# Performance work log

Hardware: AMD Instinct MI355X
Metric: run time of the kernel (lower is better)

Reference implementation:

```python
import jax, jax.numpy as jnp
import numpy as np

B, I, T = 8192, 128, 21
H1, H2, H3 = 256, 256, 128


def _init(key, shape, fan_in):
    # torch-style uniform(-1/sqrt(fan_in), 1/sqrt(fan_in))
    bound = 1.0 / np.sqrt(fan_in)
    return jax.random.uniform(key, shape, jnp.float32, -bound, bound)


def setup_inputs() -> dict:
    key = jax.random.key(0)
    ks = jax.random.split(key, 16)
    x = jax.random.normal(ks[0], (B, I, T), jnp.float32)
    d = {"x": x}
    # stacked LSTM weights (PyTorch layout: W_ih (4H, in), gate order i,f,g,o)
    d["W1_ih"] = _init(ks[1], (4 * H1, I), H1)
    d["b1_ih"] = _init(ks[2], (4 * H1,), H1)
    d["b1_hh"] = _init(ks[3], (4 * H1,), H1)
    d["W2_ih"] = _init(ks[4], (4 * H2, H1), H2)
    d["b2_ih"] = _init(ks[5], (4 * H2,), H2)
    d["b2_hh"] = _init(ks[6], (4 * H2,), H2)
    d["W3_ih"] = _init(ks[7], (4 * H3, H2), H3)
    d["b3_ih"] = _init(ks[8], (4 * H3,), H3)
    d["b3_hh"] = _init(ks[9], (4 * H3,), H3)
    d["fc1_w"] = _init(ks[10], (1, H3), H3)
    d["fc1_b"] = _init(ks[11], (1,), H3)
    d["fc2_w"] = _init(ks[12], (T, T), T)
    d["fc2_b"] = _init(ks[13], (T,), T)
    return d


def _lstm_cell_step(xt, W_ih, b_ih, b_hh):
    # single timestep with h0 = c0 = 0, so the W_hh @ h0 term vanishes
    gates = xt @ W_ih.T + (b_ih + b_hh)          # (B, 21, 4H)
    i, f, g, o = jnp.split(gates, 4, axis=-1)    # torch gate order i,f,g,o
    c = jax.nn.sigmoid(i) * jnp.tanh(g)          # f * c0 = 0
    return jax.nn.sigmoid(o) * jnp.tanh(c)


def reference(x, W1_ih, b1_ih, b1_hh, W2_ih, b2_ih, b2_hh,
              W3_ih, b3_ih, b3_hh, fc1_w, fc1_b, fc2_w, fc2_b):
    # fold the 21 independent single-step columns into the batch dim
    xt = jnp.transpose(x, (0, 2, 1))             # (B, 21, I)
    h1 = _lstm_cell_step(xt, W1_ih, b1_ih, b1_hh)   # (B, 21, H1)
    h2 = _lstm_cell_step(h1, W2_ih, b2_ih, b2_hh)   # (B, 21, H2)
    h3 = _lstm_cell_step(h2, W3_ih, b3_ih, b3_hh)   # (B, 21, H3)
    y = h3 @ fc1_w.T + fc1_b                     # (B, 21, 1)
    y = y[..., 0][:, None, :]                    # (B, 1, 21)  == x_torch
    out = y @ fc2_w.T + fc2_b                    # (B, 1, 21)
    return out
```

## Files before the change

### kernel.cpp

```cpp
#include <hip/hip_runtime.h>
#include <hip/hip_bf16.h>
#include <stdint.h>


typedef __attribute__((ext_vector_type(8))) short bf16x8;
typedef __attribute__((ext_vector_type(4))) float f32x4;

#define M_ROWS 172032
#define BATCH  8192

__device__ __forceinline__ float bf2f(unsigned short u) {
    union { unsigned int i; float f; } v; v.i = ((unsigned int)u) << 16; return v.f;
}
__device__ __forceinline__ unsigned short f2bf(float f) {
    union { float f; unsigned int i; } v; v.f = f;
    unsigned int r = v.i + 0x7fffu + ((v.i >> 16) & 1u);
    return (unsigned short)(r >> 16);
}
__device__ __forceinline__ float sigmoidf_(float x) {
    return __builtin_amdgcn_rcpf(1.0f + __expf(-x));
}
__device__ __forceinline__ float tanhf_(float x) {
    x = fminf(fmaxf(x, -20.0f), 20.0f);
    float e = __expf(-2.0f * x);
    return (1.0f - e) * __builtin_amdgcn_rcpf(1.0f + e);
}
__device__ __forceinline__ void g2l16(const unsigned short* g, unsigned short* l) {
    __builtin_amdgcn_global_load_lds(
        (const __attribute__((address_space(1))) unsigned int*)g,
        (__attribute__((address_space(3))) unsigned int*)l, 16, 0, 0);
}

__global__ __launch_bounds__(256) void k_convert(
    const float* __restrict__ src, unsigned short* __restrict__ dst, int n4)
{
    int i = blockIdx.x * 256 + threadIdx.x;
    if (i < n4) {
        float4 v = ((const float4*)src)[i];
        ushort4 o;
        o.x = f2bf(v.x); o.y = f2bf(v.y); o.z = f2bf(v.z); o.w = f2bf(v.w);
        ((ushort4*)dst)[i] = o;
    }
}

__global__ __launch_bounds__(256) void k_transpose(
    const float* __restrict__ x, unsigned short* __restrict__ xt)
{
    __shared__ unsigned short tile[128 * 22];
    const int b = blockIdx.x, tid = threadIdx.x;
    const float* xb = x + (size_t)b * 2688;
    for (int idx = tid; idx < 2688; idx += 256) {
        int i = idx / 21, t = idx - i * 21;
        tile[i * 22 + t] = f2bf(xb[idx]);
    }
    __syncthreads();
    unsigned short* xtb = xt + (size_t)b * 2688;
    for (int idx = tid; idx < 2688; idx += 256) {
        int t = idx >> 7, i = idx & 127;
        xtb[t * 128 + i] = tile[i * 22 + t];
    }
}

template<int K, int HG>
__global__ __launch_bounds__(256, 2) void k_gemm_act(
    const unsigned short* __restrict__ A,
    const unsigned short* __restrict__ W,
    const float* __restrict__ bih,
    const float* __restrict__ bhh,
    unsigned short* __restrict__ Hout)
{
    __shared__ __align__(16) unsigned short As[128 * 64];
    __shared__ __align__(16) unsigned short Ws[192 * 64];
    __shared__ float Bs[192];

    const int tid  = threadIdx.x;
    const int wave = tid >> 6;
    const int lane = tid & 63;
    const int wm = wave >> 1;
    const int wn = wave & 1;
    const int c0 = blockIdx.x * 64;
    const int r0 = blockIdx.y * 128;

    if (tid < 192) {
        int g = tid >> 6, c = tid & 63;
        int gbase = (g == 0) ? 0 : (g + 1) * HG;
        int idx = gbase + c0 + c;
        Bs[tid] = bih[idx] + bhh[idx];
    }

    f32x4 acc[3][4][2];
#pragma unroll
    for (int g = 0; g < 3; ++g)
#pragma unroll
        for (int m = 0; m < 4; ++m)
#pragma unroll
            for (int n = 0; n < 2; ++n)
                acc[g][m][n] = (f32x4){0.f, 0.f, 0.f, 0.f};

    const int l_hi = lane >> 3;
    const int l_lo = (lane & 7) * 8;

#pragma unroll
    for (int kk = 0; kk < K; kk += 64) {
        if (kk) __syncthreads();
#pragma unroll
        for (int i = 0; i < 4; ++i) {
            int row = wave * 32 + i * 8;
            g2l16(A + (size_t)(r0 + row + l_hi) * K + kk + l_lo, &As[row * 64]);
        }
#pragma unroll
        for (int i = 0; i < 6; ++i) {
            int row  = wave * 48 + i * 8;
            int lrow = row + l_hi;
            int gate = lrow >> 6;
            int n    = lrow & 63;
            int gbase = (gate == 0) ? 0 : (gate + 1) * HG;
            g2l16(W + (size_t)(gbase + c0 + n) * K + kk + l_lo, &Ws[row * 64]);
        }
        __syncthreads();

#pragma unroll
        for (int ks = 0; ks < 64; ks += 32) {
            bf16x8 af[4];
            bf16x8 bfr[3][2];
            const int koff = ks + (lane >> 4) * 8;
            const int rsel = lane & 15;
#pragma unroll
            for (int m = 0; m < 4; ++m)
                af[m] = *(const bf16x8*)&As[(wm * 64 + m * 16 + rsel) * 64 + koff];
#pragma unroll
            for (int g = 0; g < 3; ++g)
#pragma unroll
                for (int n = 0; n < 2; ++n)
                    bfr[g][n] = *(const bf16x8*)&Ws[(g * 64 + wn * 32 + n * 16 + rsel) * 64 + koff];
#pragma unroll
            for (int g = 0; g < 3; ++g)
#pragma unroll
                for (int m = 0; m < 4; ++m)
#pragma unroll
                    for (int n = 0; n < 2; ++n)
                        acc[g][m][n] = __builtin_amdgcn_mfma_f32_16x16x32_bf16(
                            af[m], bfr[g][n], acc[g][m][n], 0, 0, 0);
        }
    }

    const int quad = lane >> 4;
    const int csel = lane & 15;
#pragma unroll
    for (int m = 0; m < 4; ++m) {
#pragma unroll
        for (int n = 0; n < 2; ++n) {
            int cloc = wn * 32 + n * 16 + csel;
            float bi = Bs[cloc], bg = Bs[64 + cloc], bo = Bs[128 + cloc];
            f32x4 vi = acc[0][m][n], vg = acc[1][m][n], vo = acc[2][m][n];
#pragma unroll
            for (int r = 0; r < 4; ++r) {
                int row = r0 + wm * 64 + m * 16 + quad * 4 + r;
                float cv = sigmoidf_(vi[r] + bi) * tanhf_(vg[r] + bg);
                float h  = sigmoidf_(vo[r] + bo) * tanhf_(cv);
                Hout[(size_t)row * HG + c0 + cloc] = f2bf(h);
            }
        }
    }
}

#define FSTR 169
__global__ __launch_bounds__(256) void k_final(
    const unsigned short* __restrict__ h3,
    const float* __restrict__ fc1w,
    const float* __restrict__ fc1b,
    const float* __restrict__ fc2w,
    const float* __restrict__ fc2b,
    float* __restrict__ out)
{
    __shared__ unsigned short ht[128 * FSTR];
    __shared__ float fwl[128];
    __shared__ float yl[168];
    __shared__ float f2l[441];
    __shared__ float f2bl[21];

    const int tid = threadIdx.x;
    const int b0 = blockIdx.x * 8;

    if (tid < 128) fwl[tid] = fc1w[tid];
    for (int i = tid; i < 441; i += 256) f2l[i] = fc2w[i];
    if (tid < 21) f2bl[tid] = fc2b[tid];

    const unsigned int* hsrc = (const unsigned int*)(h3 + (size_t)b0 * 2688);
    for (int gi = tid; gi < 10752; gi += 256) {
        unsigned int v = hsrc[gi];
        int e = gi * 2;
        int task = e >> 7;
        int c = e & 127;
        ht[c * FSTR + task] = (unsigned short)(v & 0xffffu);
        ht[(c + 1) * FSTR + task] = (unsigned short)(v >> 16);
    }
    __syncthreads();

    const float f1b = fc1b[0];
    if (tid < 168) {
        float s = f1b;
#pragma unroll 8
        for (int c = 0; c < 128; ++c)
            s += fwl[c] * bf2f(ht[c * FSTR + tid]);
        yl[tid] = s;
    }
    __syncthreads();
    if (tid < 168) {
        int bloc = tid / 21;
        int tp = tid - bloc * 21;
        float s = f2bl[tp];
#pragma unroll
        for (int t = 0; t < 21; ++t)
            s += yl[bloc * 21 + t] * f2l[tp * 21 + t];
        out[(size_t)(b0 + bloc) * 21 + tp] = s;
    }
}

extern "C" void kernel_launch(void* const* d_in, const int* in_sizes, int n_in,
                              void* d_out, int out_size, void* d_ws, size_t ws_size,
                              hipStream_t stream)
{
    const float* x    = (const float*)d_in[0];
    const float* W1   = (const float*)d_in[1];
    const float* b1i  = (const float*)d_in[2];
    const float* b1h  = (const float*)d_in[3];
    const float* W2   = (const float*)d_in[4];
    const float* b2i  = (const float*)d_in[5];
    const float* b2h  = (const float*)d_in[6];
    const float* W3   = (const float*)d_in[7];
    const float* b3i  = (const float*)d_in[8];
    const float* b3h  = (const float*)d_in[9];
    const float* fc1w = (const float*)d_in[10];
    const float* fc1b = (const float*)d_in[11];
    const float* fc2w = (const float*)d_in[12];
    const float* fc2b = (const float*)d_in[13];
    float* out = (float*)d_out;

    unsigned short* Wc1 = (unsigned short*)d_ws;
    unsigned short* Wc2 = Wc1 + 131072;
    unsigned short* Wc3 = Wc2 + 262144;
    unsigned short* buf = Wc3 + 131072;

    int C = 1;
    while (C < 64 && 1048576 + (size_t)(M_ROWS / C) * 1536 > ws_size) C <<= 1;
    const int R  = M_ROWS / C;
    const int Bc = BATCH / C;

    unsigned short* xt = buf;
    unsigned short* h1 = xt + (size_t)R * 128;
    unsigned short* h2 = h1 + (size_t)R * 256;
    unsigned short* h3 = h2 + (size_t)R * 256;

    k_convert<<<128, 256, 0, stream>>>(W1, Wc1, 32768);
    k_convert<<<256, 256, 0, stream>>>(W2, Wc2, 65536);
    k_convert<<<128, 256, 0, stream>>>(W3, Wc3, 32768);

    for (int c = 0; c < C; ++c) {
        const float* xc = x + (size_t)c * Bc * 2688;
        k_transpose<<<Bc, 256, 0, stream>>>(xc, xt);
        k_gemm_act<128, 256><<<dim3(4, R / 128), 256, 0, stream>>>(xt, Wc1, b1i, b1h, h1);
        k_gemm_act<256, 256><<<dim3(4, R / 128), 256, 0, stream>>>(h1, Wc2, b2i, b2h, h2);
        k_gemm_act<256, 128><<<dim3(2, R / 128), 256, 0, stream>>>(h2, Wc3, b3i, b3h, h3);
        k_final<<<Bc / 8, 256, 0, stream>>>(h3, fc1w, fc1b, fc2w, fc2b,
                                            out + (size_t)c * Bc * 21);
    }
}
```

Before: 442.1 us.

## Fuse three LSTM layers and fc1 into one kernel with LDS-resident activations

```diff
diff --git a/kernel.cpp b/kernel.cpp
--- a/kernel.cpp
+++ b/kernel.cpp
@@ -62,77 +62,57 @@
 }
 
 template<int K, int HG>
-__global__ __launch_bounds__(256, 2) void k_gemm_act(
-    const unsigned short* __restrict__ A,
+__device__ __forceinline__ void gemm_layer(
+    const unsigned short* hin, unsigned short* hout,
     const unsigned short* __restrict__ W,
-    const float* __restrict__ bih,
-    const float* __restrict__ bhh,
-    unsigned short* __restrict__ Hout)
-{
-    __shared__ __align__(16) unsigned short As[128 * 64];
-    __shared__ __align__(16) unsigned short Ws[192 * 64];
-    __shared__ float Bs[192];
-
-    const int tid  = threadIdx.x;
-    const int wave = tid >> 6;
-    const int lane = tid & 63;
-    const int wm = wave >> 1;
-    const int wn = wave & 1;
-    const int c0 = blockIdx.x * 64;
-    const int r0 = blockIdx.y * 128;
-
-    if (tid < 192) {
-        int g = tid >> 6, c = tid & 63;
-        int gbase = (g == 0) ? 0 : (g + 1) * HG;
-        int idx = gbase + c0 + c;
-        Bs[tid] = bih[idx] + bhh[idx];
-    }
-
-    f32x4 acc[3][4][2];
-#pragma unroll
-    for (int g = 0; g < 3; ++g)
-#pragma unroll
-        for (int m = 0; m < 4; ++m)
-#pragma unroll
-            for (int n = 0; n < 2; ++n)
-                acc[g][m][n] = (f32x4){0.f, 0.f, 0.f, 0.f};
-
-    const int l_hi = lane >> 3;
-    const int l_lo = (lane & 7) * 8;
-
-#pragma unroll
-    for (int kk = 0; kk < K; kk += 64) {
-        if (kk) __syncthreads();
-#pragma unroll
-        for (int i = 0; i < 4; ++i) {
-            int row = wave * 32 + i * 8;
-            g2l16(A + (size_t)(r0 + row + l_hi) * K + kk + l_lo, &As[row * 64]);
+    const float* __restrict__ bih, const float* __restrict__ bhh,
+    int wave, int lane)
+{
+    const int quad = lane >> 4;
+    const int rsel = lane & 15;
+    const int r7   = rsel & 7;
+
+#pragma unroll
+    for (int pass = 0; pass < HG / 128; ++pass) {
+        const int c0 = pass * 128 + wave * 32;
+
+        float bias[3][2];
+#pragma unroll
+        for (int g = 0; g < 3; ++g) {
+            int gb = (g == 0) ? 0 : (g + 1) * HG;
+#pragma unroll
+            for (int n = 0; n < 2; ++n) {
+                int idx = gb + c0 + n * 16 + rsel;
+                bias[g][n] = bih[idx] + bhh[idx];
+            }
         }
-#pragma unroll
-        for (int i = 0; i < 6; ++i) {
-            int row  = wave * 48 + i * 8;
-            int lrow = row + l_hi;
-            int gate = lrow >> 6;
-            int n    = lrow & 63;
-            int gbase = (gate == 0) ? 0 : (gate + 1) * HG;
-            g2l16(W + (size_t)(gbase + c0 + n) * K + kk + l_lo, &Ws[row * 64]);
-        }
-        __syncthreads();
-
-#pragma unroll
-        for (int ks = 0; ks < 64; ks += 32) {
+
+        f32x4 acc[3][4][2];
+#pragma unroll
+        for (int g = 0; g < 3; ++g)
+#pragma unroll
+            for (int m = 0; m < 4; ++m)
+#pragma unroll
+                for (int n = 0; n < 2; ++n)
+                    acc[g][m][n] = (f32x4){0.f, 0.f, 0.f, 0.f};
+
+#pragma unroll
+        for (int ks = 0; ks < K / 32; ++ks) {
             bf16x8 af[4];
+            const int gsw = (ks * 4 + quad) ^ r7;
+#pragma unroll
+            for (int m = 0; m < 4; ++m)
+                af[m] = *(const bf16x8*)&hin[(m * 16 + rsel) * K + gsw * 8];
             bf16x8 bfr[3][2];
-            const int koff = ks + (lane >> 4) * 8;
-            const int rsel = lane & 15;
-#pragma unroll
-            for (int m = 0; m < 4; ++m)
-                af[m] = *(const bf16x8*)&As[(wm * 64 + m * 16 + rsel) * 64 + koff];
-#pragma unroll
-            for (int g = 0; g < 3; ++g)
-#pragma unroll
-                for (int n = 0; n < 2; ++n)
-                    bfr[g][n] = *(const bf16x8*)&Ws[(g * 64 + wn * 32 + n * 16 + rsel) * 64 + koff];
+#pragma unroll
+            for (int g = 0; g < 3; ++g) {
+                int gb = (g == 0) ? 0 : (g + 1) * HG;
+#pragma unroll
+                for (int n = 0; n < 2; ++n) {
+                    int col = gb + c0 + n * 16 + rsel;
+                    bfr[g][n] = *(const bf16x8*)&W[(size_t)col * K + ks * 32 + quad * 8];
+                }
+            }
 #pragma unroll
             for (int g = 0; g < 3; ++g)
 #pragma unroll
@@ -142,73 +122,91 @@
                         acc[g][m][n] = __builtin_amdgcn_mfma_f32_16x16x32_bf16(
                             af[m], bfr[g][n], acc[g][m][n], 0, 0, 0);
         }
-    }
-
-    const int quad = lane >> 4;
-    const int csel = lane & 15;
-#pragma unroll
-    for (int m = 0; m < 4; ++m) {
-#pragma unroll
-        for (int n = 0; n < 2; ++n) {
-            int cloc = wn * 32 + n * 16 + csel;
-            float bi = Bs[cloc], bg = Bs[64 + cloc], bo = Bs[128 + cloc];
-            f32x4 vi = acc[0][m][n], vg = acc[1][m][n], vo = acc[2][m][n];
-#pragma unroll
-            for (int r = 0; r < 4; ++r) {
-                int row = r0 + wm * 64 + m * 16 + quad * 4 + r;
-                float cv = sigmoidf_(vi[r] + bi) * tanhf_(vg[r] + bg);
-                float h  = sigmoidf_(vo[r] + bo) * tanhf_(cv);
-                Hout[(size_t)row * HG + c0 + cloc] = f2bf(h);
+
+#pragma unroll
+        for (int m = 0; m < 4; ++m)
+#pragma unroll
+            for (int n = 0; n < 2; ++n) {
+                f32x4 vi = acc[0][m][n], vg = acc[1][m][n], vo = acc[2][m][n];
+                int col = c0 + n * 16 + rsel;
+#pragma unroll
+                for (int r = 0; r < 4; ++r) {
+                    int row = m * 16 + quad * 4 + r;
+                    float cv = sigmoidf_(vi[r] + bias[0][n]) * tanhf_(vg[r] + bias[1][n]);
+                    float h  = sigmoidf_(vo[r] + bias[2][n]) * tanhf_(cv);
+                    int gcs = (col >> 3) ^ (row & 7);
+                    hout[row * HG + gcs * 8 + (col & 7)] = f2bf(h);
+                }
             }
+    }
+}
+
+__global__ __launch_bounds__(256, 2) void k_fused(
+    const unsigned short* __restrict__ xt,
+    const unsigned short* __restrict__ W1,
+    const unsigned short* __restrict__ W2,
+    const unsigned short* __restrict__ W3,
+    const float* __restrict__ b1i, const float* __restrict__ b1h,
+    const float* __restrict__ b2i, const float* __restrict__ b2h,
+    const float* __restrict__ b3i, const float* __restrict__ b3h,
+    const float* __restrict__ fc1w, const float* __restrict__ fc1b,
+    float* __restrict__ y)
+{
+    __shared__ __align__(16) unsigned short bufA[64 * 256];
+    __shared__ __align__(16) unsigned short bufB[64 * 256];
+    __shared__ float ypart[4][64];
+
+    const int tid  = threadIdx.x;
+    const int wave = tid >> 6;
+    const int lane = tid & 63;
+    const int r0   = blockIdx.x * 64;
+
+#pragma unroll
+    for (int i = 0; i < 4; ++i) {
+        int d   = wave * 4 + i;
+        int row = d * 4 + (lane >> 4);
+        int g   = (lane & 15) ^ (row & 7);
+        g2l16(xt + (size_t)(r0 + row) * 128 + g * 8, &bufA[d * 512]);
+    }
+    __syncthreads();
+
+    gemm_layer<128, 256>(bufA, bufB, W1, b1i, b1h, wave, lane);
+    __syncthreads();
+    gemm_layer<256, 256>(bufB, bufA, W2, b2i, b2h, wave, lane);
+    __syncthreads();
+    gemm_layer<256, 128>(bufA, bufB, W3, b3i, b3h, wave, lane);
+    __syncthreads();
+
+    {
+        int row = tid & 63, part = tid >> 6;
+        float s = 0.f;
+#pragma unroll 8
+        for (int i = 0; i < 32; ++i) {
+            int c = part * 32 + i;
+            int gcs = (c >> 3) ^ (row & 7);
+            s += fc1w[c] * bf2f(bufB[row * 128 + gcs * 8 + (c & 7)]);
         }
-    }
-}
-
-#define FSTR 169
-__global__ __launch_bounds__(256) void k_final(
-    const unsigned short* __restrict__ h3,
-    const float* __restrict__ fc1w,
-    const float* __restrict__ fc1b,
-    const float* __restrict__ fc2w,
-    const float* __restrict__ fc2b,
-    float* __restrict__ out)
-{
-    __shared__ unsigned short ht[128 * FSTR];
-    __shared__ float fwl[128];
-    __shared__ float yl[168];
-    __shared__ float f2l[441];
-    __shared__ float f2bl[21];
-
+        ypart[part][row] = s;
+        __syncthreads();
+        if (tid < 64)
+            y[r0 + tid] = fc1b[0] + ypart[0][tid] + ypart[1][tid]
+                        + ypart[2][tid] + ypart[3][tid];
+    }
+}
+
+__global__ __launch_bounds__(256) void k_fc2(
+    const float* __restrict__ y, const float* __restrict__ fc2w,
+    const float* __restrict__ fc2b, float* __restrict__ out)
+{
+    __shared__ float yl[168], f2l[441], f2bl[21];
     const int tid = threadIdx.x;
     const int b0 = blockIdx.x * 8;
-
-    if (tid < 128) fwl[tid] = fc1w[tid];
     for (int i = tid; i < 441; i += 256) f2l[i] = fc2w[i];
     if (tid < 21) f2bl[tid] = fc2b[tid];
-
-    const unsigned int* hsrc = (const unsigned int*)(h3 + (size_t)b0 * 2688);
-    for (int gi = tid; gi < 10752; gi += 256) {
-        unsigned int v = hsrc[gi];
-        int e = gi * 2;
-        int task = e >> 7;
-        int c = e & 127;
-        ht[c * FSTR + task] = (unsigned short)(v & 0xffffu);
-        ht[(c + 1) * FSTR + task] = (unsigned short)(v >> 16);
-    }
-    __syncthreads();
-
-    const float f1b = fc1b[0];
+    if (tid < 168) yl[tid] = y[(size_t)b0 * 21 + tid];
+    __syncthreads();
     if (tid < 168) {
-        float s = f1b;
-#pragma unroll 8
-        for (int c = 0; c < 128; ++c)
-            s += fwl[c] * bf2f(ht[c * FSTR + tid]);
-        yl[tid] = s;
-    }
-    __syncthreads();
-    if (tid < 168) {
-        int bloc = tid / 21;
-        int tp = tid - bloc * 21;
+        int bloc = tid / 21, tp = tid - bloc * 21;
         float s = f2bl[tp];
 #pragma unroll
         for (int t = 0; t < 21; ++t)
@@ -243,14 +241,12 @@
     unsigned short* buf = Wc3 + 131072;
 
     int C = 1;
-    while (C < 64 && 1048576 + (size_t)(M_ROWS / C) * 1536 > ws_size) C <<= 1;
+    while (C < 64 && 1048576 + (size_t)(M_ROWS / C) * 260 > ws_size) C <<= 1;
     const int R  = M_ROWS / C;
     const int Bc = BATCH / C;
 
     unsigned short* xt = buf;
-    unsigned short* h1 = xt + (size_t)R * 128;
-    unsigned short* h2 = h1 + (size_t)R * 256;
-    unsigned short* h3 = h2 + (size_t)R * 256;
+    float* y = (float*)(xt + (size_t)R * 128);
 
     k_convert<<<128, 256, 0, stream>>>(W1, Wc1, 32768);
     k_convert<<<256, 256, 0, stream>>>(W2, Wc2, 65536);
@@ -259,10 +255,10 @@
     for (int c = 0; c < C; ++c) {
         const float* xc = x + (size_t)c * Bc * 2688;
         k_transpose<<<Bc, 256, 0, stream>>>(xc, xt);
-        k_gemm_act<128, 256><<<dim3(4, R / 128), 256, 0, stream>>>(xt, Wc1, b1i, b1h, h1);
-        k_gemm_act<256, 256><<<dim3(4, R / 128), 256, 0, stream>>>(h1, Wc2, b2i, b2h, h2);
-        k_gemm_act<256, 128><<<dim3(2, R / 128), 256, 0, stream>>>(h2, Wc3, b3i, b3h, h3);
-        k_final<<<Bc / 8, 256, 0, stream>>>(h3, fc1w, fc1b, fc2w, fc2b,
-                                            out + (size_t)c * Bc * 21);
-    }
-}
+        k_fused<<<R / 64, 256, 0, stream>>>(xt, Wc1, Wc2, Wc3,
+                                            b1i, b1h, b2i, b2h, b3i, b3h,
+                                            fc1w, fc1b, y);
+        k_fc2<<<Bc / 8, 256, 0, stream>>>(y, fc2w, fc2b,
+                                          out + (size_t)c * Bc * 21);
+    }
+}
```

Result: slower. 769.2 us (+74.0%).

## Keep gate weights in registers with persistent row-tile loop and double-buffered A

Applied to the files above, without the earlier changes.

```diff
diff --git a/kernel.cpp b/kernel.cpp
--- a/kernel.cpp
+++ b/kernel.cpp
@@ -62,52 +62,46 @@
 }
 
 template<int K, int HG>
-__global__ __launch_bounds__(256, 2) void k_gemm_act(
+__global__ __launch_bounds__(256, 2) void k_gemm_reg(
     const unsigned short* __restrict__ A,
     const unsigned short* __restrict__ W,
     const float* __restrict__ bih,
     const float* __restrict__ bhh,
-    unsigned short* __restrict__ Hout)
-{
-    __shared__ __align__(16) unsigned short As[128 * 64];
-    __shared__ __align__(16) unsigned short Ws[192 * 64];
-    __shared__ float Bs[192];
+    unsigned short* __restrict__ Hout,
+    int ntiles)
+{
+    constexpr int NC = K / 64;
+    __shared__ __align__(16) unsigned short sbuf[2 * 128 * 64];
 
     const int tid  = threadIdx.x;
     const int wave = tid >> 6;
     const int lane = tid & 63;
     const int wm = wave >> 1;
     const int wn = wave & 1;
+    const int quad = lane >> 4;
+    const int rsel = lane & 15;
+    const int r7   = rsel & 7;
     const int c0 = blockIdx.x * 64;
-    const int r0 = blockIdx.y * 128;
-
-    if (tid < 192) {
-        int g = tid >> 6, c = tid & 63;
-        int gbase = (g == 0) ? 0 : (g + 1) * HG;
-        int idx = gbase + c0 + c;
-        Bs[tid] = bih[idx] + bhh[idx];
-    }
-
-    f32x4 acc[3][4][2];
-#pragma unroll
-    for (int g = 0; g < 3; ++g)
-#pragma unroll
-        for (int m = 0; m < 4; ++m)
-#pragma unroll
-            for (int n = 0; n < 2; ++n)
-                acc[g][m][n] = (f32x4){0.f, 0.f, 0.f, 0.f};
 
     const int l_hi = lane >> 3;
     const int l_lo = (lane & 7) * 8;
-
-#pragma unroll
-    for (int kk = 0; kk < K; kk += 64) {
-        if (kk) __syncthreads();
-#pragma unroll
-        for (int i = 0; i < 4; ++i) {
-            int row = wave * 32 + i * 8;
-            g2l16(A + (size_t)(r0 + row + l_hi) * K + kk + l_lo, &As[row * 64]);
-        }
+    const int swl  = ((lane & 7) ^ l_hi) * 8;
+
+    float bias[3][2];
+#pragma unroll
+    for (int g = 0; g < 3; ++g) {
+        int gb = (g == 0) ? 0 : (g + 1) * HG;
+#pragma unroll
+        for (int n = 0; n < 2; ++n) {
+            int col = gb + c0 + wn * 32 + n * 16 + rsel;
+            bias[g][n] = bih[col] + bhh[col];
+        }
+    }
+
+    bf16x8 wreg[2 * NC][3][2];
+#pragma unroll
+    for (int kc = 0; kc < NC; ++kc) {
+        const int kk = kc * 64;
 #pragma unroll
         for (int i = 0; i < 6; ++i) {
             int row  = wave * 48 + i * 8;
@@ -115,52 +109,85 @@
             int gate = lrow >> 6;
             int n    = lrow & 63;
             int gbase = (gate == 0) ? 0 : (gate + 1) * HG;
-            g2l16(W + (size_t)(gbase + c0 + n) * K + kk + l_lo, &Ws[row * 64]);
+            g2l16(W + (size_t)(gbase + c0 + n) * K + kk + l_lo, &sbuf[row * 64]);
         }
         __syncthreads();
-
-#pragma unroll
-        for (int ks = 0; ks < 64; ks += 32) {
-            bf16x8 af[4];
-            bf16x8 bfr[3][2];
-            const int koff = ks + (lane >> 4) * 8;
-            const int rsel = lane & 15;
+#pragma unroll
+        for (int ks2 = 0; ks2 < 2; ++ks2) {
+            const int koff = ks2 * 32 + quad * 8;
+#pragma unroll
+            for (int g = 0; g < 3; ++g)
+#pragma unroll
+                for (int n = 0; n < 2; ++n)
+                    wreg[kc * 2 + ks2][g][n] = *(const bf16x8*)
+                        &sbuf[(g * 64 + wn * 32 + n * 16 + rsel) * 64 + koff];
+        }
+        __syncthreads();
+    }
+
+    for (int t = blockIdx.y; t < ntiles; t += gridDim.y) {
+        const size_t r0 = (size_t)t * 128;
+
+#pragma unroll
+        for (int i = 0; i < 4; ++i) {
+            int row = wave * 32 + i * 8;
+            g2l16(A + (r0 + row + l_hi) * K + 0 + swl, &sbuf[row * 64]);
+        }
+        __syncthreads();
+
+        f32x4 acc[3][4][2];
+#pragma unroll
+        for (int g = 0; g < 3; ++g)
 #pragma unroll
             for (int m = 0; m < 4; ++m)
-                af[m] = *(const bf16x8*)&As[(wm * 64 + m * 16 + rsel) * 64 + koff];
-#pragma unroll
-            for (int g = 0; g < 3; ++g)
 #pragma unroll
                 for (int n = 0; n < 2; ++n)
-                    bfr[g][n] = *(const bf16x8*)&Ws[(g * 64 + wn * 32 + n * 16 + rsel) * 64 + koff];
-#pragma unroll
-            for (int g = 0; g < 3; ++g)
+                    acc[g][m][n] = (f32x4){0.f, 0.f, 0.f, 0.f};
+
+#pragma unroll
+        for (int c = 0; c < NC; ++c) {
+            if (c + 1 < NC) {
+                unsigned short* nb = sbuf + ((c + 1) & 1) * (128 * 64);
+#pragma unroll
+                for (int i = 0; i < 4; ++i) {
+                    int row = wave * 32 + i * 8;
+                    g2l16(A + (r0 + row + l_hi) * K + (c + 1) * 64 + swl, &nb[row * 64]);
+                }
+            }
+            const unsigned short* cb = sbuf + (c & 1) * (128 * 64);
+#pragma unroll
+            for (int ks2 = 0; ks2 < 2; ++ks2) {
+                bf16x8 af[4];
+                const int pg = ((ks2 * 4 + quad) ^ r7) * 8;
 #pragma unroll
                 for (int m = 0; m < 4; ++m)
-#pragma unroll
-                    for (int n = 0; n < 2; ++n)
-                        acc[g][m][n] = __builtin_amdgcn_mfma_f32_16x16x32_bf16(
-                            af[m], bfr[g][n], acc[g][m][n], 0, 0, 0);
-        }
-    }
-
-    const int quad = lane >> 4;
-    const int csel = lane & 15;
-#pragma unroll
-    for (int m = 0; m < 4; ++m) {
-#pragma unroll
-        for (int n = 0; n < 2; ++n) {
-            int cloc = wn * 32 + n * 16 + csel;
-            float bi = Bs[cloc], bg = Bs[64 + cloc], bo = Bs[128 + cloc];
-            f32x4 vi = acc[0][m][n], vg = acc[1][m][n], vo = acc[2][m][n];
-#pragma unroll
-            for (int r = 0; r < 4; ++r) {
-                int row = r0 + wm * 64 + m * 16 + quad * 4 + r;
-                float cv = sigmoidf_(vi[r] + bi) * tanhf_(vg[r] + bg);
-                float h  = sigmoidf_(vo[r] + bo) * tanhf_(cv);
-                Hout[(size_t)row * HG + c0 + cloc] = f2bf(h);
+                    af[m] = *(const bf16x8*)&cb[(wm * 64 + m * 16 + rsel) * 64 + pg];
+#pragma unroll
+                for (int g = 0; g < 3; ++g)
+#pragma unroll
+                    for (int m = 0; m < 4; ++m)
+#pragma unroll
+                        for (int n = 0; n < 2; ++n)
+                            acc[g][m][n] = __builtin_amdgcn_mfma_f32_16x16x32_bf16(
+                                af[m], wreg[c * 2 + ks2][g][n], acc[g][m][n], 0, 0, 0);
             }
-        }
+            __syncthreads();
+        }
+
+#pragma unroll
+        for (int m = 0; m < 4; ++m)
+#pragma unroll
+            for (int n = 0; n < 2; ++n) {
+                f32x4 vi = acc[0][m][n], vg = acc[1][m][n], vo = acc[2][m][n];
+                int col = c0 + wn * 32 + n * 16 + rsel;
+#pragma unroll
+                for (int r = 0; r < 4; ++r) {
+                    size_t row = r0 + wm * 64 + m * 16 + quad * 4 + r;
+                    float cv = sigmoidf_(vi[r] + bias[0][n]) * tanhf_(vg[r] + bias[1][n]);
+                    float h  = sigmoidf_(vo[r] + bias[2][n]) * tanhf_(cv);
+                    Hout[row * HG + col] = f2bf(h);
+                }
+            }
     }
 }
 
@@ -246,6 +273,8 @@
     while (C < 64 && 1048576 + (size_t)(M_ROWS / C) * 1536 > ws_size) C <<= 1;
     const int R  = M_ROWS / C;
     const int Bc = BATCH / C;
+    const int NT = R / 128;
+    const int NB = (NT < 336) ? NT : 336;
 
     unsigned short* xt = buf;
     unsigned short* h1 = xt + (size_t)R * 128;
@@ -259,9 +288,9 @@
     for (int c = 0; c < C; ++c) {
         const float* xc = x + (size_t)c * Bc * 2688;
         k_transpose<<<Bc, 256, 0, stream>>>(xc, xt);
-        k_gemm_act<128, 256><<<dim3(4, R / 128), 256, 0, stream>>>(xt, Wc1, b1i, b1h, h1);
-        k_gemm_act<256, 256><<<dim3(4, R / 128), 256, 0, stream>>>(h1, Wc2, b2i, b2h, h2);
-        k_gemm_act<256, 128><<<dim3(2, R / 128), 256, 0, stream>>>(h2, Wc3, b3i, b3h, h3);
+        k_gemm_reg<128, 256><<<dim3(4, NB), 256, 0, stream>>>(xt, Wc1, b1i, b1h, h1, NT);
+        k_gemm_reg<256, 256><<<dim3(4, NB), 256, 0, stream>>>(h1, Wc2, b2i, b2h, h2, NT);
+        k_gemm_reg<256, 128><<<dim3(2, NB), 256, 0, stream>>>(h2, Wc3, b3i, b3h, h3, NT);
         k_final<<<Bc / 8, 256, 0, stream>>>(h3, fc1w, fc1b, fc2w, fc2b,
                                             out + (size_t)c * Bc * 21);
     }
```

New measurement: 596.8 us. +35.0%, slower.
